# Optimization experiments

Hardware: AMD Instinct MI355X
Metric: run time of the kernel (lower is better)

Reference implementation:

```python
import jax, jax.numpy as jnp
import numpy as np

SEQ, BATCH, IN, HID, OUT = 512, 4096, 9, 64, 10


def setup_inputs() -> dict:
    key = jax.random.key(0)
    ks = jax.random.split(key, 11)
    s = 1.0 / np.sqrt(HID)
    u = lambda k, shp: jax.random.uniform(k, shp, jnp.float32, -s, s)
    return {
        "x": jax.random.normal(ks[0], (SEQ, BATCH, IN), jnp.float32),
        "W_ih0": u(ks[1], (HID, IN)),
        "W_hh0": u(ks[2], (HID, HID)),
        "b_ih0": u(ks[3], (HID,)),
        "b_hh0": u(ks[4], (HID,)),
        "W_ih1": u(ks[5], (HID, HID)),
        "W_hh1": u(ks[6], (HID, HID)),
        "b_ih1": u(ks[7], (HID,)),
        "b_hh1": u(ks[8], (HID,)),
        "W_fc": u(ks[9], (OUT, HID)),
        "b_fc": u(ks[10], (OUT,)),
    }


def _rnn_layer(x, W_ih, W_hh, b_ih, b_hh):
    # x: (seq, batch, d_in) -> (seq, batch, hid); h_t = tanh(x_t W_ih^T + b_ih + h_{t-1} W_hh^T + b_hh)
    xw = jnp.einsum('sbi,hi->sbh', x, W_ih) + (b_ih + b_hh)  # precompute input proj
    h0 = jnp.zeros((x.shape[1], W_hh.shape[0]), x.dtype)

    def step(h, xw_t):
        h = jnp.tanh(xw_t + h @ W_hh.T)
        return h, h

    _, out = jax.lax.scan(step, h0, xw)
    return out


def reference(x, W_ih0, W_hh0, b_ih0, b_hh0, W_ih1, W_hh1, b_ih1, b_hh1, W_fc, b_fc):
    h1 = _rnn_layer(x, W_ih0, W_hh0, b_ih0, b_hh0)   # (seq, batch, hid)
    h2 = _rnn_layer(h1, W_ih1, W_hh1, b_ih1, b_hh1)  # (seq, batch, hid)
    # Faithful to original quirk: rnn_out[:, -1, :] on a (seq, batch, hid) tensor
    # selects the last BATCH element for every timestep -> (seq, hid)
    feat = h2[:, -1, :]
    return feat @ W_fc.T + b_fc  # (seq, out)
```

## Files before the change

kernel.cpp:

```cpp
#include <hip/hip_runtime.h>

#define SEQn   512
#define BATCHn 4096
#define INn    9
#define HIDn   64
#define OUTn   10
#define ROW1   72
#define U2P    72

typedef __attribute__((ext_vector_type(4))) float    f32x4;
typedef __attribute__((ext_vector_type(4))) _Float16 f16x4;
typedef _Float16 half2_t __attribute__((ext_vector_type(2)));
typedef unsigned short u16;
typedef unsigned int   u32;

#define MFMA16(A,B,C) __builtin_amdgcn_mfma_f32_16x16x16f16((A),(B),(C),0,0,0)

#if __has_builtin(__builtin_amdgcn_fdot2)
#define DOT2(a,b,c) __builtin_amdgcn_fdot2((a),(b),(c),false)
#else
__device__ __forceinline__ float DOT2(half2_t a, half2_t b, float c){
    return __builtin_fmaf((float)a.x,(float)b.x, __builtin_fmaf((float)a.y,(float)b.y,c));
}
#endif
#define H2(u) __builtin_bit_cast(half2_t, (u))

__device__ __forceinline__ float tanh_pre(float x){
    float e = __builtin_amdgcn_exp2f(x);
    float r = __builtin_amdgcn_rcpf(e + 1.0f);
    return __builtin_fmaf(-2.0f, r, 1.0f);
}
__device__ __forceinline__ u16 f2h(float v){ return __builtin_bit_cast(u16, (_Float16)v); }
__device__ __forceinline__ f16x4 cvt4(f32x4 a){
    f16x4 r = {(_Float16)a.x, (_Float16)a.y, (_Float16)a.z, (_Float16)a.w};
    return r;
}

__device__ __forceinline__ void load_w16s(const float* __restrict__ W, int row, float s, half2_t* wr){
#pragma unroll
    for (int c = 0; c < 16; ++c){
        f32x4 v = *(const f32x4*)&W[row*HIDn + c*4];
        wr[2*c]   = half2_t{(_Float16)(v.x*s), (_Float16)(v.y*s)};
        wr[2*c+1] = half2_t{(_Float16)(v.z*s), (_Float16)(v.w*s)};
    }
}

__device__ __forceinline__ float dot64r8(const uint4* v, const half2_t* wr, float acc){
    float s0=acc, s1=0.f, s2=0.f, s3=0.f, s4=0.f, s5=0.f, s6=0.f, s7=0.f;
#pragma unroll
    for (int q = 0; q < 4; ++q){
        s0 = DOT2(H2(v[2*q].x),   wr[8*q+0], s0);
        s1 = DOT2(H2(v[2*q].y),   wr[8*q+1], s1);
        s2 = DOT2(H2(v[2*q].z),   wr[8*q+2], s2);
        s3 = DOT2(H2(v[2*q].w),   wr[8*q+3], s3);
        s4 = DOT2(H2(v[2*q+1].x), wr[8*q+4], s4);
        s5 = DOT2(H2(v[2*q+1].y), wr[8*q+5], s5);
        s6 = DOT2(H2(v[2*q+1].z), wr[8*q+6], s6);
        s7 = DOT2(H2(v[2*q+1].w), wr[8*q+7], s7);
    }
    return ((s0+s1)+(s2+s3)) + ((s4+s5)+(s6+s7));
}

extern "C" __global__ __launch_bounds__(256, 1)
void rnn_lastrow(const float* __restrict__ x,
                 const float* __restrict__ Wih0, const float* __restrict__ Whh0,
                 const float* __restrict__ bih0, const float* __restrict__ bhh0,
                 const float* __restrict__ Wih1, const float* __restrict__ Whh1,
                 const float* __restrict__ bih1, const float* __restrict__ bhh1,
                 const float* __restrict__ Wfc,  const float* __restrict__ bfc,
                 float* __restrict__ out)
{
    __shared__ __align__(16) u16   xl16[SEQn*16];
    __shared__ __align__(16) float u2r[64*U2P];
    __shared__ __align__(16) u16   ring1[64*ROW1];
    __shared__ __align__(16) u16   ring2[64*ROW1];
    __shared__ u32 wm[4];

    const int tid  = threadIdx.x;
    const int w    = tid >> 6;
    const int lane = tid & 63;
    const int g    = lane >> 4;
    const int n    = lane & 15;
    volatile u32* vwm = wm;
    const float K = 2.8853900817779268f;

    for (int idx = tid; idx < SEQn*16; idx += 256){
        int t = idx >> 4, j = idx & 15;
        float v = (j < INn) ? x[((long)t*BATCHn + (BATCHn-1))*INn + j] : 0.f;
        xl16[idx] = f2h(v);
    }
    for (int idx = tid; idx < 64*ROW1; idx += 256){ ring1[idx] = 0; ring2[idx] = 0; }
    if (tid < 4) wm[tid] = 0u;
    __syncthreads();

    if (w == 0){
        half2_t wr0[32], wx[5];
        load_w16s(Whh0, lane, K, wr0);
        {
            const float* wxr = Wih0 + lane*INn;
#pragma unroll
            for (int q = 0; q < 4; ++q)
                wx[q] = half2_t{(_Float16)(wxr[2*q]*K), (_Float16)(wxr[2*q+1]*K)};
            wx[4] = half2_t{(_Float16)(wxr[8]*K), (_Float16)0.f};
        }
        const float b1 = (bih0[lane] + bhh0[lane]) * K;

        for (int p = 0; p < SEQn; ++p){
            if ((p & 15) == 0 && p){
                asm volatile("s_waitcnt lgkmcnt(0)" ::: "memory");
                vwm[0] = (u32)p;
                int guard = 1 << 20;
                while ((vwm[1] + 48u < (u32)p) && --guard) __builtin_amdgcn_s_sleep(2);
                asm volatile("" ::: "memory");
            }
            const u32* xr = (const u32*)(xl16 + p*16);
            uint4 xa = *(const uint4*)xr;
            u32  xb  = xr[4];
            uint4 CUR[8];
            const uint4* hrow = (const uint4*)(ring1 + ((p-1) & 63)*ROW1);
#pragma unroll
            for (int j = 0; j < 8; ++j) CUR[j] = hrow[j];
            float u1 = b1;
            u1 = DOT2(H2(xa.x), wx[0], u1);
            u1 = DOT2(H2(xa.y), wx[1], u1);
            u1 = DOT2(H2(xa.z), wx[2], u1);
            u1 = DOT2(H2(xa.w), wx[3], u1);
            u1 = DOT2(H2(xb),   wx[4], u1);
            float y = dot64r8(CUR, wr0, u1);
            ring1[(p & 63)*ROW1 + lane] = f2h(tanh_pre(y));
        }
        asm volatile("s_waitcnt lgkmcnt(0)" ::: "memory");
        vwm[0] = (u32)SEQn;
    } else if (w == 2){
        f16x4 wi1[4][4]; f32x4 b2f[4];
#pragma unroll
        for (int r = 0; r < 4; ++r){
            f32x4 bi1 = *(const f32x4*)&bih1[16*r + 4*g];
            f32x4 bh1 = *(const f32x4*)&bhh1[16*r + 4*g];
            b2f[r] = (bi1 + bh1) * K;
#pragma unroll
            for (int c = 0; c < 4; ++c){
                f32x4 a1 = *(const f32x4*)&Wih1[(16*r + n)*HIDn + 16*c + 4*g];
                wi1[r][c] = cvt4(a1 * K);
            }
        }
        for (int b = 1; b <= 32; ++b){
            int t0 = 16*b;
            int guard = 1 << 20;
            while ((vwm[0] < (u32)t0) && --guard) __builtin_amdgcn_s_sleep(2);
            guard = 1 << 20;
            while ((vwm[2] + 64u < (u32)t0) && --guard) __builtin_amdgcn_s_sleep(2);
            asm volatile("" ::: "memory");
            f16x4 B[4];
#pragma unroll
            for (int c = 0; c < 4; ++c)
                B[c] = *(const f16x4*)&ring1[((t0-16+n) & 63)*ROW1 + 16*c + 4*g];
            f32x4 D[4];
#pragma unroll
            for (int r = 0; r < 4; ++r) D[r] = b2f[r];
#pragma unroll
            for (int c = 0; c < 4; ++c)
#pragma unroll
                for (int r = 0; r < 4; ++r)
                    D[r] = MFMA16(wi1[r][c], B[c], D[r]);
            int t = (t0 - 16 + n) & 63;
#pragma unroll
            for (int r = 0; r < 4; ++r)
                *(f32x4*)&u2r[t*U2P + 16*r + 4*g] = D[r];
            asm volatile("s_waitcnt lgkmcnt(0)" ::: "memory");
            vwm[1] = (u32)t0;
        }
    } else if (w == 1){
        half2_t wr2[32];
        load_w16s(Whh1, lane, K, wr2);
        for (int c = 0; c < SEQn; ++c){
            if ((c & 15) == 0){
                asm volatile("s_waitcnt lgkmcnt(0)" ::: "memory");
                vwm[2] = (u32)c;
                int guard = 1 << 20;
                while ((vwm[1] < (u32)(c + 16)) && --guard) __builtin_amdgcn_s_sleep(2);
                guard = 1 << 20;
                while ((vwm[3] + 48u < (u32)c) && --guard) __builtin_amdgcn_s_sleep(2);
                asm volatile("" ::: "memory");
            }
            float u2v = u2r[(c & 63)*U2P + lane];
            uint4 CUR[8];
            const uint4* hrow = (const uint4*)(ring2 + ((c-1) & 63)*ROW1);
#pragma unroll
            for (int j = 0; j < 8; ++j) CUR[j] = hrow[j];
            float y = dot64r8(CUR, wr2, u2v);
            ring2[(c & 63)*ROW1 + lane] = f2h(tanh_pre(y));
        }
        asm volatile("s_waitcnt lgkmcnt(0)" ::: "memory");
        vwm[2] = (u32)SEQn;
    } else {
        f16x4 wfcA[4]; f32x4 bfcf;
        {
            int mrow = (n < OUTn) ? n : (OUTn - 1);
#pragma unroll
            for (int c = 0; c < 4; ++c)
                wfcA[c] = cvt4(*(const f32x4*)&Wfc[mrow*HIDn + 16*c + 4*g]);
            int o0 = 4*g;
            bfcf.x = (o0+0 < OUTn) ? bfc[o0+0] : 0.f;
            bfcf.y = (o0+1 < OUTn) ? bfc[o0+1] : 0.f;
            bfcf.z = (o0+2 < OUTn) ? bfc[o0+2] : 0.f;
            bfcf.w = (o0+3 < OUTn) ? bfc[o0+3] : 0.f;
        }
        for (int b = 1; b <= 32; ++b){
            int f0 = 16*b;
            int guard = 1 << 20;
            while ((vwm[2] < (u32)f0) && --guard) __builtin_amdgcn_s_sleep(2);
            asm volatile("" ::: "memory");
            f16x4 B[4];
#pragma unroll
            for (int c = 0; c < 4; ++c)
                B[c] = *(const f16x4*)&ring2[((f0-16+n) & 63)*ROW1 + 16*c + 4*g];
            f32x4 D = bfcf;
#pragma unroll
            for (int c = 0; c < 4; ++c)
                D = MFMA16(wfcA[c], B[c], D);
            int t = f0 - 16 + n;
            float* o = out + t*OUTn + 4*g;
            if (g < 2){ o[0] = D.x; o[1] = D.y; o[2] = D.z; o[3] = D.w; }
            else if (g == 2){ o[0] = D.x; o[1] = D.y; }
            asm volatile("s_waitcnt lgkmcnt(0)" ::: "memory");
            vwm[3] = (u32)f0;
        }
    }
}

extern "C" void kernel_launch(void* const* d_in, const int* in_sizes, int n_in,
                              void* d_out, int out_size, void* d_ws, size_t ws_size,
                              hipStream_t stream){
    rnn_lastrow<<<dim3(1), dim3(256), 0, stream>>>(
        (const float*)d_in[0],
        (const float*)d_in[1], (const float*)d_in[2],
        (const float*)d_in[3], (const float*)d_in[4],
        (const float*)d_in[5], (const float*)d_in[6],
        (const float*)d_in[7], (const float*)d_in[8],
        (const float*)d_in[9], (const float*)d_in[10],
        (float*)d_out);
}
```

Measured before the change: 238.1 us.

## Replace LDS hidden-state reload with register DPP broadcast and permlane-swap reductions

The two serial recurrence waves no longer read the previous hidden state back from the LDS ring each step. Each lane keeps its own h value in a register, spreads it across lanes with DPP row broadcasts, does partial dot products against a recalibrated weight layout, and sums the partials with v_permlane16/32_swap, falling back to ds_swizzle/bpermute. The next step's x or u2 operand is also prefetched one step ahead. This removes the LDS round-trip latency from the critical serial chain, at the cost of a runtime probe of permlane semantics, inline asm with s_nop padding, and a more fragile weight-indexing scheme.

```diff
diff --git a/kernel.cpp b/kernel.cpp
--- a/kernel.cpp
+++ b/kernel.cpp
@@ -24,6 +24,8 @@
 }
 #endif
 #define H2(u) __builtin_bit_cast(half2_t, (u))
+#define BCI(f) __builtin_bit_cast(int, (f))
+#define BCF(i) __builtin_bit_cast(float, (i))
 
 __device__ __forceinline__ float tanh_pre(float x){
     float e = __builtin_amdgcn_exp2f(x);
@@ -31,34 +33,111 @@
     return __builtin_fmaf(-2.0f, r, 1.0f);
 }
 __device__ __forceinline__ u16 f2h(float v){ return __builtin_bit_cast(u16, (_Float16)v); }
+__device__ __forceinline__ float h2f(u16 u){ return (float)__builtin_bit_cast(_Float16, u); }
 __device__ __forceinline__ f16x4 cvt4(f32x4 a){
     f16x4 r = {(_Float16)a.x, (_Float16)a.y, (_Float16)a.z, (_Float16)a.w};
     return r;
 }
 
-__device__ __forceinline__ void load_w16s(const float* __restrict__ W, int row, float s, half2_t* wr){
-#pragma unroll
-    for (int c = 0; c < 16; ++c){
-        f32x4 v = *(const f32x4*)&W[row*HIDn + c*4];
-        wr[2*c]   = half2_t{(_Float16)(v.x*s), (_Float16)(v.y*s)};
-        wr[2*c+1] = half2_t{(_Float16)(v.z*s), (_Float16)(v.w*s)};
-    }
-}
-
-__device__ __forceinline__ float dot64r8(const uint4* v, const half2_t* wr, float acc){
-    float s0=acc, s1=0.f, s2=0.f, s3=0.f, s4=0.f, s5=0.f, s6=0.f, s7=0.f;
-#pragma unroll
-    for (int q = 0; q < 4; ++q){
-        s0 = DOT2(H2(v[2*q].x),   wr[8*q+0], s0);
-        s1 = DOT2(H2(v[2*q].y),   wr[8*q+1], s1);
-        s2 = DOT2(H2(v[2*q].z),   wr[8*q+2], s2);
-        s3 = DOT2(H2(v[2*q].w),   wr[8*q+3], s3);
-        s4 = DOT2(H2(v[2*q+1].x), wr[8*q+4], s4);
-        s5 = DOT2(H2(v[2*q+1].y), wr[8*q+5], s5);
-        s6 = DOT2(H2(v[2*q+1].z), wr[8*q+6], s6);
-        s7 = DOT2(H2(v[2*q+1].w), wr[8*q+7], s7);
-    }
-    return ((s0+s1)+(s2+s3)) + ((s4+s5)+(s6+s7));
+__device__ __forceinline__ void pl16(float& a, float& b){
+    asm volatile("s_nop 2\n\tv_permlane16_swap_b32 %0, %1\n\ts_nop 2" : "+v"(a), "+v"(b));
+}
+__device__ __forceinline__ void pl32(float& a, float& b){
+    asm volatile("s_nop 2\n\tv_permlane32_swap_b32 %0, %1\n\ts_nop 2" : "+v"(a), "+v"(b));
+}
+
+__device__ __forceinline__ void bcast8(float hs, u32 R[8]){
+    u32 hu = (u32)f2h(hs);
+    int d0 = __builtin_amdgcn_update_dpp(0, (int)hu, 0xA0, 0xF, 0xF, true);
+    int d1 = __builtin_amdgcn_update_dpp(0, (int)hu, 0xF5, 0xF, 0xF, true);
+    u32 base = ((u32)d0 & 0xFFFFu) | ((u32)d1 << 16);
+    R[0] = base;
+    R[1] = (u32)__builtin_amdgcn_update_dpp(0, (int)base, 0x122, 0xF, 0xF, true);
+    R[2] = (u32)__builtin_amdgcn_update_dpp(0, (int)base, 0x124, 0xF, 0xF, true);
+    R[3] = (u32)__builtin_amdgcn_update_dpp(0, (int)base, 0x126, 0xF, 0xF, true);
+    R[4] = (u32)__builtin_amdgcn_update_dpp(0, (int)base, 0x128, 0xF, 0xF, true);
+    R[5] = (u32)__builtin_amdgcn_update_dpp(0, (int)base, 0x12A, 0xF, 0xF, true);
+    R[6] = (u32)__builtin_amdgcn_update_dpp(0, (int)base, 0x12C, 0xF, 0xF, true);
+    R[7] = (u32)__builtin_amdgcn_update_dpp(0, (int)base, 0x12E, 0xF, 0xF, true);
+}
+
+__device__ __forceinline__ void probe_conv(int lane, int& mode, int& y16, int& y32){
+    float pa = (float)lane, pb = 1000.f + (float)lane;
+    pl16(pa, pb);
+    float a0  = BCF(__builtin_amdgcn_readlane(BCI(pa), 0));
+    float a16 = BCF(__builtin_amdgcn_readlane(BCI(pa), 16));
+    float a32 = BCF(__builtin_amdgcn_readlane(BCI(pa), 32));
+    float a48 = BCF(__builtin_amdgcn_readlane(BCI(pa), 48));
+    int c16;
+    if      (a0==1016.f && a16==16.f   && a32==1048.f && a48==48.f)   c16 = 0;
+    else if (a0==0.f    && a16==1000.f && a32==32.f   && a48==1032.f) c16 = 1;
+    else c16 = 2;
+    float qa = (float)lane, qb = 1000.f + (float)lane;
+    pl32(qa, qb);
+    float b0  = BCF(__builtin_amdgcn_readlane(BCI(qa), 0));
+    float b32 = BCF(__builtin_amdgcn_readlane(BCI(qa), 32));
+    int c32;
+    if      (b0==1032.f && b32==32.f)   c32 = 0;
+    else if (b0==0.f    && b32==1000.f) c32 = 1;
+    else c32 = 2;
+    mode = (c16 <= 1 && c32 <= 1) ? 0 : 1;
+    y16 = (c16 == 1); y32 = (c32 == 1);
+}
+
+__device__ __forceinline__ void load_wcal(const float* __restrict__ W, int n, float s,
+                                          int mode, int y16, int y32, int lane,
+                                          half2_t wr[4][8]){
+    u32 Rp[8];
+    bcast8((float)lane, Rp);
+#pragma unroll
+    for (int m = 0; m < 8; ++m){
+        int ke = ((int)h2f((u16)(Rp[m] & 0xFFFFu))) & 63;
+        int ko = ((int)h2f((u16)(Rp[m] >> 16)))     & 63;
+#pragma unroll
+        for (int j = 0; j < 4; ++j){
+            int jj = (mode == 0) ? (j ^ y16 ^ (y32 << 1)) : j;
+            const float* row = W + (n + 16*jj)*HIDn;
+            wr[j][m] = half2_t{(_Float16)(row[ke]*s), (_Float16)(row[ko]*s)};
+        }
+    }
+}
+
+__device__ __forceinline__ float matvec_rr(float hs, const half2_t wr[4][8],
+                                           int mode, int lane){
+    u32 R[8];
+    bcast8(hs, R);
+    float a[4];
+#pragma unroll
+    for (int j = 0; j < 4; ++j){
+        float sA = DOT2(H2(R[0]), wr[j][0], 0.f);
+        sA = DOT2(H2(R[1]), wr[j][1], sA);
+        sA = DOT2(H2(R[2]), wr[j][2], sA);
+        sA = DOT2(H2(R[3]), wr[j][3], sA);
+        float sB = DOT2(H2(R[4]), wr[j][4], 0.f);
+        sB = DOT2(H2(R[5]), wr[j][5], sB);
+        sB = DOT2(H2(R[6]), wr[j][6], sB);
+        sB = DOT2(H2(R[7]), wr[j][7], sB);
+        a[j] = sA + sB;
+    }
+    if (mode == 0){
+        pl16(a[1], a[0]); float S1 = a[1] + a[0];
+        pl16(a[3], a[2]); float S2 = a[3] + a[2];
+        pl32(S2, S1);
+        return S1 + S2;
+    } else {
+#pragma unroll
+        for (int j = 0; j < 4; ++j){
+            int t = __builtin_amdgcn_ds_swizzle(BCI(a[j]), 0x401F);
+            a[j] += BCF(t);
+        }
+        int g = (lane >> 4) & 3;
+        float s01 = (g & 1) ? a[1] : a[0];
+        float s23 = (g & 1) ? a[3] : a[2];
+        float vs  = (g & 2) ? s23 : s01;
+        float vc  = (g & 2) ? s01 : s23;
+        int t = __builtin_amdgcn_ds_bpermute((lane ^ 32) << 2, BCI(vc));
+        return vs + BCF(t);
+    }
 }
 
 extern "C" __global__ __launch_bounds__(256, 1)
@@ -94,8 +173,11 @@
     __syncthreads();
 
     if (w == 0){
-        half2_t wr0[32], wx[5];
-        load_w16s(Whh0, lane, K, wr0);
+        int mode, y16, y32;
+        probe_conv(lane, mode, y16, y32);
+        half2_t wr0[4][8];
+        load_wcal(Whh0, n, K, mode, y16, y32, lane, wr0);
+        half2_t wx[5];
         {
             const float* wxr = Wih0 + lane*INn;
 #pragma unroll
@@ -104,6 +186,9 @@
             wx[4] = half2_t{(_Float16)(wxr[8]*K), (_Float16)0.f};
         }
         const float b1 = (bih0[lane] + bhh0[lane]) * K;
+        float hs = 0.f;
+        uint4 xa_c; u32 xb_c;
+        { const u32* xr = (const u32*)(xl16); xa_c = *(const uint4*)xr; xb_c = xr[4]; }
 
         for (int p = 0; p < SEQn; ++p){
             if ((p & 15) == 0 && p){
@@ -113,21 +198,19 @@
                 while ((vwm[1] + 48u < (u32)p) && --guard) __builtin_amdgcn_s_sleep(2);
                 asm volatile("" ::: "memory");
             }
-            const u32* xr = (const u32*)(xl16 + p*16);
-            uint4 xa = *(const uint4*)xr;
-            u32  xb  = xr[4];
-            uint4 CUR[8];
-            const uint4* hrow = (const uint4*)(ring1 + ((p-1) & 63)*ROW1);
-#pragma unroll
-            for (int j = 0; j < 8; ++j) CUR[j] = hrow[j];
+            const u32* xr = (const u32*)(xl16 + ((p+1) & (SEQn-1))*16);
+            uint4 xa_n = *(const uint4*)xr;
+            u32  xb_n  = xr[4];
             float u1 = b1;
-            u1 = DOT2(H2(xa.x), wx[0], u1);
-            u1 = DOT2(H2(xa.y), wx[1], u1);
-            u1 = DOT2(H2(xa.z), wx[2], u1);
-            u1 = DOT2(H2(xa.w), wx[3], u1);
-            u1 = DOT2(H2(xb),   wx[4], u1);
-            float y = dot64r8(CUR, wr0, u1);
-            ring1[(p & 63)*ROW1 + lane] = f2h(tanh_pre(y));
+            u1 = DOT2(H2(xa_c.x), wx[0], u1);
+            u1 = DOT2(H2(xa_c.y), wx[1], u1);
+            u1 = DOT2(H2(xa_c.z), wx[2], u1);
+            u1 = DOT2(H2(xa_c.w), wx[3], u1);
+            u1 = DOT2(H2(xb_c),   wx[4], u1);
+            float z = matvec_rr(hs, wr0, mode, lane);
+            hs = tanh_pre(z + u1);
+            ring1[(p & 63)*ROW1 + lane] = f2h(hs);
+            xa_c = xa_n; xb_c = xb_n;
         }
         asm volatile("s_waitcnt lgkmcnt(0)" ::: "memory");
         vwm[0] = (u32)SEQn;
@@ -171,25 +254,29 @@
             vwm[1] = (u32)t0;
         }
     } else if (w == 1){
-        half2_t wr2[32];
-        load_w16s(Whh1, lane, K, wr2);
+        int mode, y16, y32;
+        probe_conv(lane, mode, y16, y32);
+        half2_t wr1[4][8];
+        load_wcal(Whh1, n, K, mode, y16, y32, lane, wr1);
+        float hs2 = 0.f;
+        float u2c = 0.f;
         for (int c = 0; c < SEQn; ++c){
             if ((c & 15) == 0){
                 asm volatile("s_waitcnt lgkmcnt(0)" ::: "memory");
                 vwm[2] = (u32)c;
+                u32 need = (c + 17 <= SEQn) ? (u32)(c + 17) : (u32)SEQn;
                 int guard = 1 << 20;
-                while ((vwm[1] < (u32)(c + 16)) && --guard) __builtin_amdgcn_s_sleep(2);
+                while ((vwm[1] < need) && --guard) __builtin_amdgcn_s_sleep(2);
                 guard = 1 << 20;
                 while ((vwm[3] + 48u < (u32)c) && --guard) __builtin_amdgcn_s_sleep(2);
                 asm volatile("" ::: "memory");
+                if (c == 0) u2c = u2r[lane];
             }
-            float u2v = u2r[(c & 63)*U2P + lane];
-            uint4 CUR[8];
-            const uint4* hrow = (const uint4*)(ring2 + ((c-1) & 63)*ROW1);
-#pragma unroll
-            for (int j = 0; j < 8; ++j) CUR[j] = hrow[j];
-            float y = dot64r8(CUR, wr2, u2v);
-            ring2[(c & 63)*ROW1 + lane] = f2h(tanh_pre(y));
+            float u2n = u2r[((c+1) & 63)*U2P + lane];
+            float z = matvec_rr(hs2, wr1, mode, lane);
+            hs2 = tanh_pre(z + u2c);
+            ring2[(c & 63)*ROW1 + lane] = f2h(hs2);
+            u2c = u2n;
         }
         asm volatile("s_waitcnt lgkmcnt(0)" ::: "memory");
         vwm[2] = (u32)SEQn;
```

After: 273.7 us. 1.15x slower.

## Fuse both recurrent layers into one wavefront with skewed interleaving

Applied to the files above, without the earlier changes.

Moves the layer-1 and layer-2 recurrences onto a single wavefront. Layer 2 runs LAG=33 steps behind layer 1, and each iteration computes one step of each, so the two independent dependency chains hide each other's LDS and dot-product latency. The next x row is also prefetched, and the spin-wait sleep is shortened. The cost is higher register pressure, since both weight sets are held in registers, and a more intricate prologue/epilogue with changed wavefront roles and synchronisation.

```diff
diff --git a/kernel.cpp b/kernel.cpp
--- a/kernel.cpp
+++ b/kernel.cpp
@@ -5,6 +5,7 @@
 #define INn    9
 #define HIDn   64
 #define OUTn   10
+#define LAG    33
 #define ROW1   72
 #define U2P    72
 
@@ -94,8 +95,9 @@
     __syncthreads();
 
     if (w == 0){
-        half2_t wr0[32], wx[5];
+        half2_t wr0[32], wr2[32], wx[5];
         load_w16s(Whh0, lane, K, wr0);
+        load_w16s(Whh1, lane, K, wr2);
         {
             const float* wxr = Wih0 + lane*INn;
 #pragma unroll
@@ -105,33 +107,99 @@
         }
         const float b1 = (bih0[lane] + bhh0[lane]) * K;
 
-        for (int p = 0; p < SEQn; ++p){
+        uint4 C1[8], C2[8];
+        uint4 xa_c; u32 xb_c;
+        { const u32* xr = (const u32*)(xl16); xa_c = *(const uint4*)xr; xb_c = xr[4]; }
+
+        for (int p = 0; p < LAG; ++p){
             if ((p & 15) == 0 && p){
                 asm volatile("s_waitcnt lgkmcnt(0)" ::: "memory");
                 vwm[0] = (u32)p;
+            }
+            const uint4* hr = (const uint4*)(ring1 + ((p-1) & 63)*ROW1);
+#pragma unroll
+            for (int j = 0; j < 8; ++j) C1[j] = hr[j];
+            float u1 = b1;
+            u1 = DOT2(H2(xa_c.x), wx[0], u1);
+            u1 = DOT2(H2(xa_c.y), wx[1], u1);
+            u1 = DOT2(H2(xa_c.z), wx[2], u1);
+            u1 = DOT2(H2(xa_c.w), wx[3], u1);
+            u1 = DOT2(H2(xb_c),   wx[4], u1);
+            const u32* xr = (const u32*)(xl16 + ((p+1) & (SEQn-1))*16);
+            uint4 xa_n = *(const uint4*)xr; u32 xb_n = xr[4];
+            float y1 = dot64r8(C1, wr0, u1);
+            ring1[(p & 63)*ROW1 + lane] = f2h(tanh_pre(y1));
+            xa_c = xa_n; xb_c = xb_n;
+        }
+        float u2c;
+        {
+            int guard = 1 << 20;
+            while ((vwm[1] < 16u) && --guard) __builtin_amdgcn_s_sleep(2);
+            asm volatile("" ::: "memory");
+            u2c = u2r[lane];
+            const uint4* hr = (const uint4*)(ring2 + 63*ROW1);
+#pragma unroll
+            for (int j = 0; j < 8; ++j) C2[j] = hr[j];
+        }
+        for (int i = LAG; i < SEQn; ++i){
+            const int p = i, c = i - LAG;
+            if ((i & 15) == 0){
+                asm volatile("s_waitcnt lgkmcnt(0)" ::: "memory");
+                vwm[0] = (u32)i;
+                vwm[2] = (u32)c;
                 int guard = 1 << 20;
-                while ((vwm[1] + 48u < (u32)p) && --guard) __builtin_amdgcn_s_sleep(2);
+                while ((vwm[1] < (u32)(i - 16)) && --guard) __builtin_amdgcn_s_sleep(1);
+                guard = 1 << 20;
+                while ((vwm[3] + 48u < (u32)c) && --guard) __builtin_amdgcn_s_sleep(1);
                 asm volatile("" ::: "memory");
             }
-            const u32* xr = (const u32*)(xl16 + p*16);
-            uint4 xa = *(const uint4*)xr;
-            u32  xb  = xr[4];
-            uint4 CUR[8];
-            const uint4* hrow = (const uint4*)(ring1 + ((p-1) & 63)*ROW1);
-#pragma unroll
-            for (int j = 0; j < 8; ++j) CUR[j] = hrow[j];
+            {
+                const uint4* hr = (const uint4*)(ring1 + ((p-1) & 63)*ROW1);
+#pragma unroll
+                for (int j = 0; j < 8; ++j) C1[j] = hr[j];
+            }
             float u1 = b1;
-            u1 = DOT2(H2(xa.x), wx[0], u1);
-            u1 = DOT2(H2(xa.y), wx[1], u1);
-            u1 = DOT2(H2(xa.z), wx[2], u1);
-            u1 = DOT2(H2(xa.w), wx[3], u1);
-            u1 = DOT2(H2(xb),   wx[4], u1);
-            float y = dot64r8(CUR, wr0, u1);
-            ring1[(p & 63)*ROW1 + lane] = f2h(tanh_pre(y));
+            u1 = DOT2(H2(xa_c.x), wx[0], u1);
+            u1 = DOT2(H2(xa_c.y), wx[1], u1);
+            u1 = DOT2(H2(xa_c.z), wx[2], u1);
+            u1 = DOT2(H2(xa_c.w), wx[3], u1);
+            u1 = DOT2(H2(xb_c),   wx[4], u1);
+            float y2 = dot64r8(C2, wr2, 0.f) + u2c;
+            ring2[(c & 63)*ROW1 + lane] = f2h(tanh_pre(y2));
+            const u32* xr = (const u32*)(xl16 + ((p+1) & (SEQn-1))*16);
+            uint4 xa_n = *(const uint4*)xr; u32 xb_n = xr[4];
+            float y1 = dot64r8(C1, wr0, u1);
+            ring1[(p & 63)*ROW1 + lane] = f2h(tanh_pre(y1));
+            {
+                const uint4* hr = (const uint4*)(ring2 + (c & 63)*ROW1);
+#pragma unroll
+                for (int j = 0; j < 8; ++j) C2[j] = hr[j];
+            }
+            u2c = u2r[((c+1) & 63)*U2P + lane];
+            xa_c = xa_n; xb_c = xb_n;
         }
         asm volatile("s_waitcnt lgkmcnt(0)" ::: "memory");
         vwm[0] = (u32)SEQn;
-    } else if (w == 2){
+        for (int c = SEQn - LAG; c < SEQn; ++c){
+            if ((c & 15) == 0){
+                asm volatile("s_waitcnt lgkmcnt(0)" ::: "memory");
+                vwm[2] = (u32)c;
+                int guard = 1 << 20;
+                while ((vwm[1] < (u32)(c + 16)) && --guard) __builtin_amdgcn_s_sleep(1);
+                guard = 1 << 20;
+                while ((vwm[3] + 48u < (u32)c) && --guard) __builtin_amdgcn_s_sleep(1);
+                asm volatile("" ::: "memory");
+            }
+            float u2v = u2r[(c & 63)*U2P + lane];
+            float y2 = dot64r8(C2, wr2, 0.f) + u2v;
+            ring2[(c & 63)*ROW1 + lane] = f2h(tanh_pre(y2));
+            const uint4* hr = (const uint4*)(ring2 + (c & 63)*ROW1);
+#pragma unroll
+            for (int j = 0; j < 8; ++j) C2[j] = hr[j];
+        }
+        asm volatile("s_waitcnt lgkmcnt(0)" ::: "memory");
+        vwm[2] = (u32)SEQn;
+    } else if (w == 1){
         f16x4 wi1[4][4]; f32x4 b2f[4];
 #pragma unroll
         for (int r = 0; r < 4; ++r){
@@ -170,30 +238,7 @@
             asm volatile("s_waitcnt lgkmcnt(0)" ::: "memory");
             vwm[1] = (u32)t0;
         }
-    } else if (w == 1){
-        half2_t wr2[32];
-        load_w16s(Whh1, lane, K, wr2);
-        for (int c = 0; c < SEQn; ++c){
-            if ((c & 15) == 0){
-                asm volatile("s_waitcnt lgkmcnt(0)" ::: "memory");
-                vwm[2] = (u32)c;
-                int guard = 1 << 20;
-                while ((vwm[1] < (u32)(c + 16)) && --guard) __builtin_amdgcn_s_sleep(2);
-                guard = 1 << 20;
-                while ((vwm[3] + 48u < (u32)c) && --guard) __builtin_amdgcn_s_sleep(2);
-                asm volatile("" ::: "memory");
-            }
-            float u2v = u2r[(c & 63)*U2P + lane];
-            uint4 CUR[8];
-            const uint4* hrow = (const uint4*)(ring2 + ((c-1) & 63)*ROW1);
-#pragma unroll
-            for (int j = 0; j < 8; ++j) CUR[j] = hrow[j];
-            float y = dot64r8(CUR, wr2, u2v);
-            ring2[(c & 63)*ROW1 + lane] = f2h(tanh_pre(y));
-        }
-        asm volatile("s_waitcnt lgkmcnt(0)" ::: "memory");
-        vwm[2] = (u32)SEQn;
-    } else {
+    } else if (w == 2){
         f16x4 wfcA[4]; f32x4 bfcf;
         {
             int mrow = (n < OUTn) ? n : (OUTn - 1);
```

After: 291.5 us. 1.22x slower.

## Move layer-0 input projection to MFMA producer wave and prefetch projected inputs

Applied to the files above, without the earlier changes.

Wave 3 now also computes the layer-0 input projection (x·W_ih0 plus bias) for 16 timesteps at a time with MFMA, writing it to a shared-memory ring. The serial recurrence waves then only add a prefetched scalar, loaded one step ahead, to the hidden-state dot product. This takes the x staging prologue and the per-step input dot products off the critical recurrence chain. The trade-off is extra cross-wave synchronisation, finer sleep granularity in the spin-waits, and wave 3 interleaving FC batches with projection batches, which could delay either.

```diff
diff --git a/kernel.cpp b/kernel.cpp
--- a/kernel.cpp
+++ b/kernel.cpp
@@ -45,8 +45,8 @@
     }
 }
 
-__device__ __forceinline__ float dot64r8(const uint4* v, const half2_t* wr, float acc){
-    float s0=acc, s1=0.f, s2=0.f, s3=0.f, s4=0.f, s5=0.f, s6=0.f, s7=0.f;
+__device__ __forceinline__ float dot64z(const uint4* v, const half2_t* wr){
+    float s0=0.f, s1=0.f, s2=0.f, s3=0.f, s4=0.f, s5=0.f, s6=0.f, s7=0.f;
 #pragma unroll
     for (int q = 0; q < 4; ++q){
         s0 = DOT2(H2(v[2*q].x),   wr[8*q+0], s0);
@@ -70,11 +70,11 @@
                  const float* __restrict__ Wfc,  const float* __restrict__ bfc,
                  float* __restrict__ out)
 {
-    __shared__ __align__(16) u16   xl16[SEQn*16];
+    __shared__ __align__(16) float u1r[64*U2P];
     __shared__ __align__(16) float u2r[64*U2P];
     __shared__ __align__(16) u16   ring1[64*ROW1];
     __shared__ __align__(16) u16   ring2[64*ROW1];
-    __shared__ u32 wm[4];
+    __shared__ u32 wm[8];
 
     const int tid  = threadIdx.x;
     const int w    = tid >> 6;
@@ -84,53 +84,68 @@
     volatile u32* vwm = wm;
     const float K = 2.8853900817779268f;
 
-    for (int idx = tid; idx < SEQn*16; idx += 256){
-        int t = idx >> 4, j = idx & 15;
-        float v = (j < INn) ? x[((long)t*BATCHn + (BATCHn-1))*INn + j] : 0.f;
-        xl16[idx] = f2h(v);
-    }
     for (int idx = tid; idx < 64*ROW1; idx += 256){ ring1[idx] = 0; ring2[idx] = 0; }
-    if (tid < 4) wm[tid] = 0u;
+    if (tid < 8) wm[tid] = 0u;
     __syncthreads();
 
     if (w == 0){
-        half2_t wr0[32], wx[5];
+        half2_t wr0[32];
         load_w16s(Whh0, lane, K, wr0);
-        {
-            const float* wxr = Wih0 + lane*INn;
-#pragma unroll
-            for (int q = 0; q < 4; ++q)
-                wx[q] = half2_t{(_Float16)(wxr[2*q]*K), (_Float16)(wxr[2*q+1]*K)};
-            wx[4] = half2_t{(_Float16)(wxr[8]*K), (_Float16)0.f};
-        }
-        const float b1 = (bih0[lane] + bhh0[lane]) * K;
+        uint4 C1[8];
+        float u1c = 0.f;
 
         for (int p = 0; p < SEQn; ++p){
-            if ((p & 15) == 0 && p){
+            if ((p & 15) == 0){
                 asm volatile("s_waitcnt lgkmcnt(0)" ::: "memory");
                 vwm[0] = (u32)p;
+                if (p){
+                    int guard = 1 << 20;
+                    while ((vwm[1] + 48u < (u32)p) && --guard) __builtin_amdgcn_s_sleep(1);
+                }
+                u32 need = (p + 32 <= SEQn) ? (u32)(p + 32) : (u32)SEQn;
                 int guard = 1 << 20;
-                while ((vwm[1] + 48u < (u32)p) && --guard) __builtin_amdgcn_s_sleep(2);
+                while ((vwm[4] < need) && --guard) __builtin_amdgcn_s_sleep(1);
                 asm volatile("" ::: "memory");
-            }
-            const u32* xr = (const u32*)(xl16 + p*16);
-            uint4 xa = *(const uint4*)xr;
-            u32  xb  = xr[4];
-            uint4 CUR[8];
-            const uint4* hrow = (const uint4*)(ring1 + ((p-1) & 63)*ROW1);
-#pragma unroll
-            for (int j = 0; j < 8; ++j) CUR[j] = hrow[j];
-            float u1 = b1;
-            u1 = DOT2(H2(xa.x), wx[0], u1);
-            u1 = DOT2(H2(xa.y), wx[1], u1);
-            u1 = DOT2(H2(xa.z), wx[2], u1);
-            u1 = DOT2(H2(xa.w), wx[3], u1);
-            u1 = DOT2(H2(xb),   wx[4], u1);
-            float y = dot64r8(CUR, wr0, u1);
-            ring1[(p & 63)*ROW1 + lane] = f2h(tanh_pre(y));
+                if (p == 0) u1c = u1r[lane];
+            }
+            const uint4* hr = (const uint4*)(ring1 + ((p-1) & 63)*ROW1);
+#pragma unroll
+            for (int j = 0; j < 8; ++j) C1[j] = hr[j];
+            float u1n = u1r[((p+1) & 63)*U2P + lane];
+            float y1 = dot64z(C1, wr0) + u1c;
+            ring1[(p & 63)*ROW1 + lane] = f2h(tanh_pre(y1));
+            u1c = u1n;
         }
         asm volatile("s_waitcnt lgkmcnt(0)" ::: "memory");
         vwm[0] = (u32)SEQn;
+    } else if (w == 1){
+        half2_t wr2[32];
+        load_w16s(Whh1, lane, K, wr2);
+        uint4 C2[8];
+        float u2c = 0.f;
+
+        for (int c = 0; c < SEQn; ++c){
+            if ((c & 15) == 0){
+                asm volatile("s_waitcnt lgkmcnt(0)" ::: "memory");
+                vwm[2] = (u32)c;
+                u32 need = (c + 32 <= SEQn) ? (u32)(c + 32) : (u32)SEQn;
+                int guard = 1 << 20;
+                while ((vwm[1] < need) && --guard) __builtin_amdgcn_s_sleep(1);
+                guard = 1 << 20;
+                while ((vwm[3] + 48u < (u32)c) && --guard) __builtin_amdgcn_s_sleep(1);
+                asm volatile("" ::: "memory");
+                if (c == 0) u2c = u2r[lane];
+            }
+            const uint4* hr = (const uint4*)(ring2 + ((c-1) & 63)*ROW1);
+#pragma unroll
+            for (int j = 0; j < 8; ++j) C2[j] = hr[j];
+            float u2n = u2r[((c+1) & 63)*U2P + lane];
+            float y2 = dot64z(C2, wr2) + u2c;
+            ring2[(c & 63)*ROW1 + lane] = f2h(tanh_pre(y2));
+            u2c = u2n;
+        }
+        asm volatile("s_waitcnt lgkmcnt(0)" ::: "memory");
+        vwm[2] = (u32)SEQn;
     } else if (w == 2){
         f16x4 wi1[4][4]; f32x4 b2f[4];
 #pragma unroll
@@ -170,30 +185,22 @@
             asm volatile("s_waitcnt lgkmcnt(0)" ::: "memory");
             vwm[1] = (u32)t0;
         }
-    } else if (w == 1){
-        half2_t wr2[32];
-        load_w16s(Whh1, lane, K, wr2);
-        for (int c = 0; c < SEQn; ++c){
-            if ((c & 15) == 0){
-                asm volatile("s_waitcnt lgkmcnt(0)" ::: "memory");
-                vwm[2] = (u32)c;
-                int guard = 1 << 20;
-                while ((vwm[1] < (u32)(c + 16)) && --guard) __builtin_amdgcn_s_sleep(2);
-                guard = 1 << 20;
-                while ((vwm[3] + 48u < (u32)c) && --guard) __builtin_amdgcn_s_sleep(2);
-                asm volatile("" ::: "memory");
-            }
-            float u2v = u2r[(c & 63)*U2P + lane];
-            uint4 CUR[8];
-            const uint4* hrow = (const uint4*)(ring2 + ((c-1) & 63)*ROW1);
-#pragma unroll
-            for (int j = 0; j < 8; ++j) CUR[j] = hrow[j];
-            float y = dot64r8(CUR, wr2, u2v);
-            ring2[(c & 63)*ROW1 + lane] = f2h(tanh_pre(y));
-        }
-        asm volatile("s_waitcnt lgkmcnt(0)" ::: "memory");
-        vwm[2] = (u32)SEQn;
     } else {
+        f16x4 wA[4]; f32x4 b1f[4];
+#pragma unroll
+        for (int r = 0; r < 4; ++r){
+            f32x4 bi = *(const f32x4*)&bih0[16*r + 4*g];
+            f32x4 bh = *(const f32x4*)&bhh0[16*r + 4*g];
+            b1f[r] = (bi + bh) * K;
+            f16x4 e;
+            const float* row = Wih0 + (16*r + n)*INn;
+            int k0 = 4*g;
+            e.x = (_Float16)((k0+0 < INn) ? row[k0+0]*K : 0.f);
+            e.y = (_Float16)((k0+1 < INn) ? row[k0+1]*K : 0.f);
+            e.z = (_Float16)((k0+2 < INn) ? row[k0+2]*K : 0.f);
+            e.w = (_Float16)((k0+3 < INn) ? row[k0+3]*K : 0.f);
+            wA[r] = e;
+        }
         f16x4 wfcA[4]; f32x4 bfcf;
         {
             int mrow = (n < OUTn) ? n : (OUTn - 1);
@@ -206,11 +213,7 @@
             bfcf.z = (o0+2 < OUTn) ? bfc[o0+2] : 0.f;
             bfcf.w = (o0+3 < OUTn) ? bfc[o0+3] : 0.f;
         }
-        for (int b = 1; b <= 32; ++b){
-            int f0 = 16*b;
-            int guard = 1 << 20;
-            while ((vwm[2] < (u32)f0) && --guard) __builtin_amdgcn_s_sleep(2);
-            asm volatile("" ::: "memory");
+        auto fcbatch = [&](int f0){
             f16x4 B[4];
 #pragma unroll
             for (int c = 0; c < 4; ++c)
@@ -225,6 +228,48 @@
             else if (g == 2){ o[0] = D.x; o[1] = D.y; }
             asm volatile("s_waitcnt lgkmcnt(0)" ::: "memory");
             vwm[3] = (u32)f0;
+        };
+
+        int fc_next = 1;
+        for (int b = 1; b <= 32; ++b){
+            int t0 = 16*b;
+            int guard = 1 << 22;
+            while ((vwm[0] + 46u < (u32)t0) && --guard){
+                if (fc_next <= 32 && vwm[2] >= (u32)(16*fc_next)){
+                    asm volatile("" ::: "memory");
+                    fcbatch(16*fc_next); ++fc_next;
+                } else __builtin_amdgcn_s_sleep(1);
+            }
+            asm volatile("" ::: "memory");
+            const float* xrow = x + ((long)(t0-16+n)*BATCHn + (BATCHn-1))*INn;
+            f16x4 B;
+            if (g < 2){
+                f32x4 v = *(const f32x4*)&xrow[4*g];
+                B = cvt4(v);
+            } else if (g == 2){
+                B = f16x4{(_Float16)xrow[8], (_Float16)0.f, (_Float16)0.f, (_Float16)0.f};
+            } else {
+                B = f16x4{(_Float16)0.f, (_Float16)0.f, (_Float16)0.f, (_Float16)0.f};
+            }
+            f32x4 D[4];
+#pragma unroll
+            for (int r = 0; r < 4; ++r) D[r] = MFMA16(wA[r], B, b1f[r]);
+            int t = (t0 - 16 + n) & 63;
+#pragma unroll
+            for (int r = 0; r < 4; ++r)
+                *(f32x4*)&u1r[t*U2P + 16*r + 4*g] = D[r];
+            asm volatile("s_waitcnt lgkmcnt(0)" ::: "memory");
+            vwm[4] = (u32)t0;
+            while (fc_next <= 32 && vwm[2] >= (u32)(16*fc_next)){
+                asm volatile("" ::: "memory");
+                fcbatch(16*fc_next); ++fc_next;
+            }
+        }
+        while (fc_next <= 32){
+            int guard = 1 << 20;
+            while ((vwm[2] < (u32)(16*fc_next)) && --guard) __builtin_amdgcn_s_sleep(2);
+            asm volatile("" ::: "memory");
+            fcbatch(16*fc_next); ++fc_next;
         }
     }
 }
```

Measured after the change: 246.5 us. 3.5% more time.
